# Kernel tuning notes

Measured on AMD Instinct MI355X. Metric: run time of the kernel, lower is better.

## Reference

```python
import jax, jax.numpy as jnp
import numpy as np

BATCH = 16384
XD = 64      # x_dim
AD = 16      # a_dim
NC = 8       # number of constraints
PEN = 10.0   # relax_penalty
DELTA = 1.0  # class-K coefficient
ITERS = 250  # FISTA iterations for the dual QP (converges to OSQP solution)


def _cbf_forward(a_des, x, A, B, Qc, cc, dc):
    """Batched CBF-QP safety filter.

    Constraints: g_i(x) = 0.5 x^T Qc_i x + cc_i^T x - dc_i  (g_i <= 0 is safe)
    Barrier:     h_i(x) = -g_i(x),  grad_h = -(Qc_i x + cc_i)
    QP:  min ||a - a_des||^2 + PEN * ||s||^2
         s.t. Lg_h a >= -Lf_h - DELTA*h - s,  s >= 0
    Solved exactly (to FISTA tolerance) via the dual:
         min_{lam>=0} 0.5 lam^T M lam - lam^T q,
    with z = [a; s], H = diag(2*1_AD, 2*PEN*1_NC), z = z0 + H^{-1} G^T lam.
    """
    bsz = a_des.shape[0]
    # constraint values and gradients (the 'autograd jacobian' in the original)
    g_x = 0.5 * jnp.einsum('bi,mij,bj->bm', x, Qc, x) + x @ cc.T - dc[None, :]
    h_x = -g_x                                              # [B, NC]
    grad_h = -(jnp.einsum('mij,bj->bmi', Qc, x) + cc[None])  # [B, NC, XD]
    # Lie derivatives
    Lf_h = jnp.einsum('bmi,bij,bj->bm', grad_h, A, x)        # [B, NC]
    Lg_h = jnp.einsum('bmi,bia->bma', grad_h, B)             # [B, NC, AD]
    bvec = -Lf_h - DELTA * h_x                               # rhs: Lg_h a + s >= bvec

    # dual QP setup: G z >= c, G = [[Lg_h, I],[0, I]], c = [bvec; 0]
    Im = jnp.broadcast_to(jnp.eye(NC, dtype=a_des.dtype), (bsz, NC, NC))
    Gtop = jnp.concatenate([Lg_h, Im], axis=2)                    # [B, NC, AD+NC]
    Gbot = jnp.concatenate([jnp.zeros((bsz, NC, AD), a_des.dtype), Im], axis=2)
    G = jnp.concatenate([Gtop, Gbot], axis=1)                     # [B, 2NC, AD+NC]
    dinv = jnp.concatenate([0.5 * jnp.ones(AD, a_des.dtype),
                            jnp.ones(NC, a_des.dtype) / (2.0 * PEN)])
    Mmat = jnp.einsum('bkn,n,bln->bkl', G, dinv, G)               # [B, 2NC, 2NC]
    q = jnp.concatenate([bvec - jnp.einsum('bma,ba->bm', Lg_h, a_des),
                         jnp.zeros((bsz, NC), a_des.dtype)], axis=1)

    # step size 1/L, L = max eigenvalue of M (not differentiated)
    L = jax.lax.stop_gradient(jnp.linalg.eigvalsh(Mmat)[..., -1]) + 1e-6
    t = (1.0 / L)[:, None]

    lam0 = jnp.zeros((bsz, 2 * NC), a_des.dtype)

    def step(carry, _):
        lam, y, tk = carry
        grad = jnp.einsum('bkl,bl->bk', Mmat, y) - q
        lam_new = jnp.maximum(y - t * grad, 0.0)
        tk1 = 0.5 * (1.0 + jnp.sqrt(1.0 + 4.0 * tk * tk))
        y_new = lam_new + ((tk - 1.0) / tk1) * (lam_new - lam)
        return (lam_new, y_new, tk1), None

    (lam, _, _), _ = jax.lax.scan(step, (lam0, lam0, jnp.float32(1.0)), None, length=ITERS)

    # primal recovery: a = a_des + 0.5 * Lg_h^T lam_top
    a_safe = a_des + 0.5 * jnp.einsum('bma,bm->ba', Lg_h, lam[:, :NC])
    return a_safe


def setup_inputs() -> dict:
    key = jax.random.key(0)
    ks = jax.random.split(key, 7)
    a_des = jax.random.normal(ks[0], (BATCH, AD), jnp.float32)
    x = jax.random.normal(ks[1], (BATCH, XD), jnp.float32)
    A = jax.random.normal(ks[2], (BATCH, XD, XD), jnp.float32) * 0.05
    B = jax.random.normal(ks[3], (BATCH, XD, AD), jnp.float32) * 0.1
    R = jax.random.normal(ks[4], (NC, XD, XD), jnp.float32) * 0.05
    Qc = R + jnp.swapaxes(R, 1, 2)  # symmetric quadratic constraint Hessians
    cc = jax.random.normal(ks[5], (NC, XD), jnp.float32) * 0.1
    dc = jax.random.uniform(ks[6], (NC,), jnp.float32) + 0.5
    return {"a_des": a_des, "x": x, "A": A, "B": B, "Qc": Qc, "cc": cc, "dc": dc}


def reference(a_des, x, A, B, Qc, cc, dc):
    return _cbf_forward(a_des, x, A, B, Qc, cc, dc)
```

## Files before the change

kernel.cpp:

```cpp
#include <hip/hip_runtime.h>
#include <cstddef>

#define NBATCH 16384

struct Betas {
  float b[250];
  static constexpr double csqrt(double x) {
    double g = x > 1.0 ? x : 1.0;
    for (int i = 0; i < 64; ++i) g = 0.5 * (g + x / g);
    return g;
  }
  constexpr Betas() : b{} {
    double tk = 1.0;
    for (int i = 0; i < 250; ++i) {
      double tk1 = 0.5 * (1.0 + csqrt(1.0 + 4.0 * tk * tk));
      b[i] = (float)((tk - 1.0) / tk1);
      tk = tk1;
    }
  }
};
__device__ constexpr Betas BETAS{};

template <int CTRL>
__device__ __forceinline__ float fdpp(float v) {
  return __int_as_float(
      __builtin_amdgcn_mov_dpp(__float_as_int(v), CTRL, 0xF, 0xF, true));
}
__device__ __forceinline__ float rowsum16(float p) {
  p += fdpp<0x121>(p);
  p += fdpp<0x122>(p);
  p += fdpp<0x124>(p);
  p += fdpp<0x128>(p);
  return p;
}

__global__ __launch_bounds__(256) void cbf_k1_gh(
    const float* __restrict__ Qc, const float* __restrict__ cc,
    const float* __restrict__ X, float* __restrict__ gh) {
  __shared__ float qt[128 * 64];
  __shared__ float cct[128];
  const int tid = threadIdx.x;
  const int e   = tid & 63;
  const int rc  = tid >> 6;
  const int b0  = (blockIdx.x & 255) * 64;
  const int r0  = (blockIdx.x >> 8) * 128;

  {
    const float4* qsrc = (const float4*)(Qc + (size_t)r0 * 64);
    float4* qdst = (float4*)qt;
#pragma unroll
    for (int i = 0; i < 8; ++i) qdst[i * 256 + tid] = qsrc[i * 256 + tid];
    if (tid < 32) ((float4*)cct)[tid] = ((const float4*)(cc + r0))[tid];
  }

  float4 xr[16];
  {
    const float4* xp = (const float4*)(X + (size_t)(b0 + e) * 64);
#pragma unroll
    for (int c = 0; c < 16; ++c) xr[c] = xp[c];
  }
  __syncthreads();

  const int rcu = __builtin_amdgcn_readfirstlane(rc);
  const float* qrow = qt + rcu * 32 * 64;
  float* ob = gh + (size_t)(b0 + e) * 512 + r0 + rcu * 32;

#pragma unroll 2
  for (int rg = 0; rg < 8; ++rg) {
    float o[4];
#pragma unroll
    for (int j = 0; j < 4; ++j) {
      const float4* w = (const float4*)(qrow + (rg * 4 + j) * 64);
      float a0 = 0.f, a1 = 0.f;
#pragma unroll
      for (int c = 0; c < 16; ++c) {
        float4 wv = w[c];
        a0 = fmaf(wv.x, xr[c].x, a0);
        a1 = fmaf(wv.y, xr[c].y, a1);
        a0 = fmaf(wv.z, xr[c].z, a0);
        a1 = fmaf(wv.w, xr[c].w, a1);
      }
      o[j] = a0 + a1 + cct[rcu * 32 + rg * 4 + j];
    }
    *(float4*)(ob + rg * 4) = *(const float4*)o;
  }
}

#define XOFF  0
#define BVOFF 64
#define BOFF  72
#define GHOFF (72 + 1024)
#define LGOFF (1096 + 544)
#define AXOFF (1640 + 160)
#define ESTR  (1800 + 64)

__global__ __launch_bounds__(256) void cbf_k2_setup(
    const float* __restrict__ X, const float* __restrict__ Abat,
    const float* __restrict__ Bbat, const float* __restrict__ cc,
    const float* __restrict__ dc, const float* __restrict__ a_des,
    const float* __restrict__ gh, float* __restrict__ S_ws,
    float* __restrict__ LgT_ws, float* __restrict__ qu_ws) {
  __shared__ float smem[4 * ESTR];
  const int tid  = threadIdx.x;
  const int sub  = tid >> 6;
  const int lane = tid & 63;
  const int b    = blockIdx.x * 4 + sub;
  float* sm = smem + sub * ESTR;

  const float xi = X[(size_t)b * 64 + lane];
  sm[XOFF + lane] = xi;
  {
    const float4* bp = (const float4*)(Bbat + (size_t)b * 1024);
#pragma unroll
    for (int n = 0; n < 4; ++n) {
      float4 v = bp[n * 64 + lane];
      *(float4*)&sm[BOFF + n * 256 + lane * 4] = v;
    }
  }
  {
    const float4* gp = (const float4*)(gh + (size_t)b * 512);
    float4 g0 = gp[lane];
    float4 g1 = gp[64 + lane];
    const int f0 = lane * 4, f1 = 256 + lane * 4;
    *(float4*)&sm[GHOFF + (f0 >> 6) * 68 + (f0 & 63)] = g0;
    *(float4*)&sm[GHOFF + (f1 >> 6) * 68 + (f1 & 63)] = g1;
  }
  __syncthreads();

  {
    const float4* ap = (const float4*)(Abat + (size_t)b * 4096);
    const int cg = lane & 15;
    const int rg = lane >> 4;
    const float4 xv = *(const float4*)&sm[XOFF + cg * 4];
#pragma unroll
    for (int n = 0; n < 16; ++n) {
      float4 av = ap[n * 64 + lane];
      float p = av.x * xv.x + av.y * xv.y + av.z * xv.z + av.w * xv.w;
      p = rowsum16(p);
      if (cg == 0) sm[AXOFF + n * 4 + rg] = p;
    }
  }
  __syncthreads();

  {
    const int m  = lane >> 3;
    const int ig = lane & 7;
    const float4 ghA = *(const float4*)&sm[GHOFF + m * 68 + ig * 8];
    const float4 ghB = *(const float4*)&sm[GHOFF + m * 68 + ig * 8 + 4];
    const float4 xA  = *(const float4*)&sm[XOFF + ig * 8];
    const float4 xB  = *(const float4*)&sm[XOFF + ig * 8 + 4];
    const float4 axA = *(const float4*)&sm[AXOFF + ig * 8];
    const float4 axB = *(const float4*)&sm[AXOFF + ig * 8 + 4];
    const float4 ccA = *(const float4*)(cc + m * 64 + ig * 8);
    const float4 ccB = *(const float4*)(cc + m * 64 + ig * 8 + 4);
    float p1 = ghA.x * xA.x + ghA.y * xA.y + ghA.z * xA.z + ghA.w * xA.w
             + ghB.x * xB.x + ghB.y * xB.y + ghB.z * xB.z + ghB.w * xB.w;
    float p2 = ghA.x * axA.x + ghA.y * axA.y + ghA.z * axA.z + ghA.w * axA.w
             + ghB.x * axB.x + ghB.y * axB.y + ghB.z * axB.z + ghB.w * axB.w;
    float p3 = ccA.x * xA.x + ccA.y * xA.y + ccA.z * xA.z + ccA.w * xA.w
             + ccB.x * xB.x + ccB.y * xB.y + ccB.z * xB.z + ccB.w * xB.w;
    p1 += __shfl_xor(p1, 1); p1 += __shfl_xor(p1, 2); p1 += __shfl_xor(p1, 4);
    p2 += __shfl_xor(p2, 1); p2 += __shfl_xor(p2, 2); p2 += __shfl_xor(p2, 4);
    p3 += __shfl_xor(p3, 1); p3 += __shfl_xor(p3, 2); p3 += __shfl_xor(p3, 4);
    if (ig == 0) {
      sm[BVOFF + m] = p2 + 0.5f * (p1 + p3) - dc[m];
    }
  }

  const int mq  = lane >> 3;
  const int ap2 = lane & 7;
  {
    float acc0 = 0.f, acc1 = 0.f;
#pragma unroll
    for (int c = 0; c < 16; ++c) {
      float4 gv = *(const float4*)&sm[GHOFF + mq * 68 + 4 * c];
#pragma unroll
      for (int n = 0; n < 4; ++n) {
        float2 bv2 = *(const float2*)&sm[BOFF + (4 * c + n) * 16 + 2 * ap2];
        float gvn = (n == 0) ? gv.x : ((n == 1) ? gv.y : ((n == 2) ? gv.z : gv.w));
        acc0 = fmaf(gvn, bv2.x, acc0);
        acc1 = fmaf(gvn, bv2.y, acc1);
      }
    }
    const float lg0 = -acc0, lg1 = -acc1;
    LgT_ws[(size_t)b * 128 + (2 * ap2) * 8 + mq]     = lg0;
    LgT_ws[(size_t)b * 128 + (2 * ap2 + 1) * 8 + mq] = lg1;
    sm[LGOFF + mq * 20 + 2 * ap2]     = lg0;
    sm[LGOFF + mq * 20 + 2 * ap2 + 1] = lg1;
  }
  __syncthreads();

  const int kq = lane >> 3;
  const int lq = lane & 7;
  {
    float s = 0.f;
#pragma unroll
    for (int c = 0; c < 4; ++c) {
      float4 ka = *(const float4*)&sm[LGOFF + kq * 20 + 4 * c];
      float4 la = *(const float4*)&sm[LGOFF + lq * 20 + 4 * c];
      s = fmaf(ka.x, la.x, s);
      s = fmaf(ka.y, la.y, s);
      s = fmaf(ka.z, la.z, s);
      s = fmaf(ka.w, la.w, s);
    }
    S_ws[(size_t)b * 64 + kq * 8 + lq] = 0.5f * s;
  }

  {
    float2 ad2 = *(const float2*)(a_des + (size_t)b * 16 + 2 * lq);
    float2 kg  = *(const float2*)&sm[LGOFF + kq * 20 + 2 * lq];
    float p = kg.x * ad2.x + kg.y * ad2.y;
    p += __shfl_xor(p, 1);
    p += __shfl_xor(p, 2);
    p += __shfl_xor(p, 4);
    if (lq == 0) qu_ws[(size_t)b * 8 + kq] = sm[BVOFF + kq] - p;
  }
}

__global__ __launch_bounds__(256) void cbf_k3_fista(
    const float* __restrict__ S_ws, const float* __restrict__ qu_ws,
    const float* __restrict__ LgT_ws, const float* __restrict__ a_des,
    float* __restrict__ out) {
  const int gt = blockIdx.x * 256 + threadIdx.x;
  const int e  = gt >> 2;
  const int q  = gt & 3;

  const float4* Sp = (const float4*)(S_ws + (size_t)e * 64);
  const float4 sl0 = Sp[q * 2],       sl1 = Sp[q * 2 + 1];
  const float4 sh0 = Sp[(q + 4) * 2], sh1 = Sp[(q + 4) * 2 + 1];
  const float qu_lo = qu_ws[(size_t)e * 8 + q];
  const float qu_hi = qu_ws[(size_t)e * 8 + q + 4];

#define MV(ylo, yhi, alo, ahi) do {                                          \
    float b0 = fdpp<0x00>(ylo), b1 = fdpp<0x55>(ylo);                        \
    float b2 = fdpp<0xAA>(ylo), b3 = fdpp<0xFF>(ylo);                        \
    float b4 = fdpp<0x00>(yhi), b5 = fdpp<0x55>(yhi);                        \
    float b6 = fdpp<0xAA>(yhi), b7 = fdpp<0xFF>(yhi);                        \
    float t0 = sl0.x * b0, t1 = sl0.y * b1;                                  \
    t0 = fmaf(sl0.z, b2, t0); t1 = fmaf(sl0.w, b3, t1);                      \
    t0 = fmaf(sl1.x, b4, t0); t1 = fmaf(sl1.y, b5, t1);                      \
    t0 = fmaf(sl1.z, b6, t0); t1 = fmaf(sl1.w, b7, t1);                      \
    alo = t0 + t1;                                                           \
    float u0 = sh0.x * b0, u1 = sh0.y * b1;                                  \
    u0 = fmaf(sh0.z, b2, u0); u1 = fmaf(sh0.w, b3, u1);                      \
    u0 = fmaf(sh1.x, b4, u0); u1 = fmaf(sh1.y, b5, u1);                      \
    u0 = fmaf(sh1.z, b6, u0); u1 = fmaf(sh1.w, b7, u1);                      \
    ahi = u0 + u1;                                                           \
  } while (0)

  float vl = 1.f, vh = 1.f, svl, svh;
#pragma unroll 4
  for (int it = 0; it < 40; ++it) {
    MV(vl, vh, svl, svh);
    float am = fmaxf(fabsf(svl), fabsf(svh));
    am = fmaxf(am, fdpp<0xB1>(am));
    am = fmaxf(am, fdpp<0x4E>(am));
    float r = 1.f / fmaxf(am, 1e-30f);
    vl = svl * r; vh = svh * r;
  }
  MV(vl, vh, svl, svh);
  float num = vl * svl + vh * svh;
  float den = vl * vl + vh * vh;
  num += fdpp<0xB1>(num); den += fdpp<0xB1>(den);
  num += fdpp<0x4E>(num); den += fdpp<0x4E>(den);
  float mu = fmaxf((num / fmaxf(den, 1e-30f)) * 1.001f, 0.f);
  const float lmax = 0.5f * ((0.1f + mu) + sqrtf(fmaf(mu, mu, 0.01f)));
  const float t = 1.0f / (lmax + 1e-6f);

  float yul = 0.f, yuh = 0.f, yvl = 0.f, yvh = 0.f;
  float lul = 0.f, luh = 0.f, lvl_ = 0.f, lvh = 0.f;
#pragma unroll 5
  for (int it = 0; it < 250; ++it) {
    const float beta = BETAS.b[it];
    const float wl = 0.05f * (yul + yvl);
    const float wh = 0.05f * (yuh + yvh);
    float al, ah;
    MV(yul, yuh, al, ah);
    const float gul = al + wl - qu_lo;
    const float guh = ah + wh - qu_hi;
    const float lunl = fmaxf(fmaf(-t, gul, yul), 0.f);
    const float lunh = fmaxf(fmaf(-t, guh, yuh), 0.f);
    const float lvnl = fmaxf(fmaf(-t, wl, yvl), 0.f);
    const float lvnh = fmaxf(fmaf(-t, wh, yvh), 0.f);
    yul = fmaf(beta, lunl - lul, lunl); lul = lunl;
    yuh = fmaf(beta, lunh - luh, lunh); luh = lunh;
    yvl = fmaf(beta, lvnl - lvl_, lvnl); lvl_ = lvnl;
    yvh = fmaf(beta, lvnh - lvh, lvnh); lvh = lvnh;
  }
#undef MV

  const float l0 = fdpp<0x00>(lul), l1 = fdpp<0x55>(lul);
  const float l2 = fdpp<0xAA>(lul), l3 = fdpp<0xFF>(lul);
  const float l4 = fdpp<0x00>(luh), l5 = fdpp<0x55>(luh);
  const float l6 = fdpp<0xAA>(luh), l7 = fdpp<0xFF>(luh);
  const float4* Lp = (const float4*)(LgT_ws + (size_t)e * 128 + q * 32);
  const float4 ad  = *(const float4*)(a_des + (size_t)e * 16 + q * 4);
  float o[4];
#pragma unroll
  for (int j = 0; j < 4; ++j) {
    float4 ga = Lp[j * 2], gb = Lp[j * 2 + 1];
    float s = ga.x * l0 + ga.y * l1 + ga.z * l2 + ga.w * l3
            + gb.x * l4 + gb.y * l5 + gb.z * l6 + gb.w * l7;
    o[j] = 0.5f * s;
  }
  float4 ov;
  ov.x = ad.x + o[0]; ov.y = ad.y + o[1];
  ov.z = ad.z + o[2]; ov.w = ad.w + o[3];
  *(float4*)(out + (size_t)e * 16 + q * 4) = ov;
}

extern "C" void kernel_launch(void* const* d_in, const int* in_sizes, int n_in,
                              void* d_out, int out_size, void* d_ws, size_t ws_size,
                              hipStream_t stream) {
  (void)in_sizes; (void)n_in; (void)out_size; (void)ws_size;
  const float* a_des = (const float*)d_in[0];
  const float* x     = (const float*)d_in[1];
  const float* A     = (const float*)d_in[2];
  const float* B     = (const float*)d_in[3];
  const float* Qc    = (const float*)d_in[4];
  const float* cc    = (const float*)d_in[5];
  const float* dc    = (const float*)d_in[6];
  float* out = (float*)d_out;

  float* gh  = (float*)d_ws;
  float* S   = gh  + (size_t)NBATCH * 512;
  float* LgT = S   + (size_t)NBATCH * 64;
  float* qu  = LgT + (size_t)NBATCH * 128;

  hipLaunchKernelGGL(cbf_k1_gh, dim3(1024), dim3(256), 0, stream, Qc, cc, x, gh);
  hipLaunchKernelGGL(cbf_k2_setup, dim3(4096), dim3(256), 0, stream,
                     x, A, B, cc, dc, a_des, gh, S, LgT, qu);
  hipLaunchKernelGGL(cbf_k3_fista, dim3(256), dim3(256), 0, stream,
                     S, qu, LgT, a_des, out);
}
```

Measured before the change: 477.1 us.

## Retile Qc-times-x GEMM kernel with 8x8 register outer-product blocking

Rewrites the first kernel, which computes the constraint gradients (x·Qcᵀ + cc), as a shared-memory tiled GEMM. Both x and Qc tiles of 128 rows are staged in LDS with a row padding of 65 floats. Each thread then accumulates an 8x8 output tile from float4 loads, so it does more FMAs per LDS read than before, when each thread kept one x row in registers. The padding leaves float4 LDS accesses misaligned, which may be split into smaller accesses or cause bank conflicts. The register tile also raises register pressure, and the grid is halved.

```diff
diff --git a/kernel.cpp b/kernel.cpp
--- a/kernel.cpp
+++ b/kernel.cpp
@@ -37,52 +37,65 @@
 __global__ __launch_bounds__(256) void cbf_k1_gh(
     const float* __restrict__ Qc, const float* __restrict__ cc,
     const float* __restrict__ X, float* __restrict__ gh) {
-  __shared__ float qt[128 * 64];
+  __shared__ float xt[128 * 65];
+  __shared__ float qt[128 * 65];
   __shared__ float cct[128];
   const int tid = threadIdx.x;
-  const int e   = tid & 63;
-  const int rc  = tid >> 6;
-  const int b0  = (blockIdx.x & 255) * 64;
-  const int r0  = (blockIdx.x >> 8) * 128;
-
-  {
-    const float4* qsrc = (const float4*)(Qc + (size_t)r0 * 64);
-    float4* qdst = (float4*)qt;
-#pragma unroll
-    for (int i = 0; i < 8; ++i) qdst[i * 256 + tid] = qsrc[i * 256 + tid];
-    if (tid < 32) ((float4*)cct)[tid] = ((const float4*)(cc + r0))[tid];
-  }
-
-  float4 xr[16];
-  {
-    const float4* xp = (const float4*)(X + (size_t)(b0 + e) * 64);
-#pragma unroll
-    for (int c = 0; c < 16; ++c) xr[c] = xp[c];
-  }
+  const int b0 = (blockIdx.x >> 2) * 128;
+  const int r0 = (blockIdx.x & 3) * 128;
+
+#pragma unroll
+  for (int i = 0; i < 8; ++i) {
+    const int g   = i * 256 + tid;
+    const int row = g >> 4;
+    const int c4  = g & 15;
+    float4 v = *(const float4*)(X  + (size_t)(b0 + row) * 64 + c4 * 4);
+    float4 w = *(const float4*)(Qc + (size_t)(r0 + row) * 64 + c4 * 4);
+    *(float4*)&xt[row * 65 + c4 * 4] = v;
+    *(float4*)&qt[row * 65 + c4 * 4] = w;
+  }
+  if (tid < 128) cct[tid] = cc[r0 + tid];
   __syncthreads();
 
-  const int rcu = __builtin_amdgcn_readfirstlane(rc);
-  const float* qrow = qt + rcu * 32 * 64;
-  float* ob = gh + (size_t)(b0 + e) * 512 + r0 + rcu * 32;
-
+  const int w  = tid >> 6;
+  const int bw = (w & 1) * 64;
+  const int rw = (w >> 1) * 64;
+  const int bi = (tid & 7) * 8;
+  const int rj = ((tid >> 3) & 7) * 8;
+  const float* xb = xt + (bw + bi) * 65;
+  const float* qb = qt + (rw + rj) * 65;
+
+  float acc[8][8] = {};
 #pragma unroll 2
-  for (int rg = 0; rg < 8; ++rg) {
-    float o[4];
-#pragma unroll
-    for (int j = 0; j < 4; ++j) {
-      const float4* w = (const float4*)(qrow + (rg * 4 + j) * 64);
-      float a0 = 0.f, a1 = 0.f;
-#pragma unroll
-      for (int c = 0; c < 16; ++c) {
-        float4 wv = w[c];
-        a0 = fmaf(wv.x, xr[c].x, a0);
-        a1 = fmaf(wv.y, xr[c].y, a1);
-        a0 = fmaf(wv.z, xr[c].z, a0);
-        a1 = fmaf(wv.w, xr[c].w, a1);
+  for (int cg = 0; cg < 16; ++cg) {
+    float4 xa[8], qa[8];
+#pragma unroll
+    for (int i = 0; i < 8; ++i) xa[i] = *(const float4*)&xb[i * 65 + cg * 4];
+#pragma unroll
+    for (int j = 0; j < 8; ++j) qa[j] = *(const float4*)&qb[j * 65 + cg * 4];
+#pragma unroll
+    for (int i = 0; i < 8; ++i)
+#pragma unroll
+      for (int j = 0; j < 8; ++j) {
+        acc[i][j] = fmaf(xa[i].x, qa[j].x, acc[i][j]);
+        acc[i][j] = fmaf(xa[i].y, qa[j].y, acc[i][j]);
+        acc[i][j] = fmaf(xa[i].z, qa[j].z, acc[i][j]);
+        acc[i][j] = fmaf(xa[i].w, qa[j].w, acc[i][j]);
       }
-      o[j] = a0 + a1 + cct[rcu * 32 + rg * 4 + j];
-    }
-    *(float4*)(ob + rg * 4) = *(const float4*)o;
+  }
+
+  float cc8[8];
+  *(float4*)&cc8[0] = *(const float4*)&cct[rw + rj];
+  *(float4*)&cc8[4] = *(const float4*)&cct[rw + rj + 4];
+  const int gr = r0 + rw + rj;
+#pragma unroll
+  for (int i = 0; i < 8; ++i) {
+    float o[8];
+#pragma unroll
+    for (int j = 0; j < 8; ++j) o[j] = acc[i][j] + cc8[j];
+    float* dst = gh + (size_t)(b0 + bw + bi + i) * 512 + gr;
+    *(float4*)dst       = *(const float4*)&o[0];
+    *(float4*)(dst + 4) = *(const float4*)&o[4];
   }
 }
 
@@ -327,7 +340,7 @@
   float* LgT = S   + (size_t)NBATCH * 64;
   float* qu  = LgT + (size_t)NBATCH * 128;
 
-  hipLaunchKernelGGL(cbf_k1_gh, dim3(1024), dim3(256), 0, stream, Qc, cc, x, gh);
+  hipLaunchKernelGGL(cbf_k1_gh, dim3(512), dim3(256), 0, stream, Qc, cc, x, gh);
   hipLaunchKernelGGL(cbf_k2_setup, dim3(4096), dim3(256), 0, stream,
                      x, A, B, cc, dc, a_des, gh, S, LgT, qu);
   hipLaunchKernelGGL(cbf_k3_fista, dim3(256), dim3(256), 0, stream,
```

New measurement: 488.8 us. 1.02x slower.
